# Kernel tuning notes

Hardware: AMD Instinct MI355X
Metric: run time of the kernel (lower is better)

The kernel has to match this reference:

```python
import jax, jax.numpy as jnp
import numpy as np

D = 2048  # input_size
H = 2048  # hidden_size
B = 8192  # batch


def _xavier(key, shape):
    fan_out, fan_in = shape
    limit = float(np.sqrt(6.0 / (fan_in + fan_out)))
    return jax.random.uniform(key, shape, jnp.float32, -limit, limit)


def setup_inputs() -> dict:
    key = jax.random.key(0)
    ks = jax.random.split(key, 20)
    inp = {
        "x": jax.random.normal(ks[0], (B, D), jnp.float32),
        "h0": jax.random.normal(ks[1], (B, H), jnp.float32),
        "c0": jax.random.normal(ks[2], (B, H), jnp.float32),
    }
    names_i = ["W_ii", "W_if", "W_ig", "W_io"]
    names_h = ["W_hi", "W_hf", "W_hg", "W_ho"]
    for i, n in enumerate(names_i):
        inp[n] = _xavier(ks[3 + i], (H, D))
        inp["b" + n[1:]] = jnp.zeros((H,), jnp.float32)
    for i, n in enumerate(names_h):
        inp[n] = _xavier(ks[7 + i], (H, H))
        inp["b" + n[1:]] = jnp.zeros((H,), jnp.float32)
    return inp


def reference(x, h0, c0,
              W_ii, b_ii, W_hi, b_hi,
              W_if, b_if, W_hf, b_hf,
              W_ig, b_ig, W_hg, b_hg,
              W_io, b_io, W_ho, b_ho):
    # Fuse the 8 small GEMMs into two [*, 4H] GEMMs (gate order: i, f, g, o).
    Wx = jnp.concatenate([W_ii, W_if, W_ig, W_io], axis=0)   # [4H, D]
    Wh = jnp.concatenate([W_hi, W_hf, W_hg, W_ho], axis=0)   # [4H, H]
    b = jnp.concatenate([b_ii + b_hi, b_if + b_hf, b_ig + b_hg, b_io + b_ho])
    gates = x @ Wx.T + h0 @ Wh.T + b                         # [B, 4H]
    i_t = jax.nn.sigmoid(gates[:, 0 * H:1 * H])
    f_t = jax.nn.sigmoid(gates[:, 1 * H:2 * H])
    g_t = jnp.tanh(gates[:, 2 * H:3 * H])
    o_t = jax.nn.sigmoid(gates[:, 3 * H:4 * H])
    c_t = f_t * c0 + i_t * g_t
    h_t = o_t * jnp.tanh(c_t)
    return (h_t, c_t)
```

## Files before the change

### kernel.cpp

```cpp
#include <hip/hip_runtime.h>
#include <hip/hip_bf16.h>
#include <cstdint>
#include <cstddef>

#define BATCH 8192
#define DIN   2048
#define HID   2048
#define KDIM  4096
#define NDIM  8192
#define MDIM  8192
#define BH    16777216
#define NT    64

typedef unsigned short u16;
typedef __bf16 bf16x8 __attribute__((ext_vector_type(8)));
typedef float  f32x4  __attribute__((ext_vector_type(4)));

__device__ __forceinline__ u16 f2bf(float f) {
    union { float f; unsigned u; } a; a.f = f;
    unsigned u = a.u;
    unsigned r = u + 0x7FFFu + ((u >> 16) & 1u);
    return (u16)(r >> 16);
}
__device__ __forceinline__ float lo16(unsigned v) {
    union { unsigned u; float f; } a; a.u = v << 16; return a.f;
}
__device__ __forceinline__ float hi16(unsigned v) {
    union { unsigned u; float f; } a; a.u = v & 0xFFFF0000u; return a.f;
}
__device__ __forceinline__ void unpack8(uint4 p, float* f) {
    f[0] = lo16(p.x); f[1] = hi16(p.x);
    f[2] = lo16(p.y); f[3] = hi16(p.y);
    f[4] = lo16(p.z); f[5] = hi16(p.z);
    f[6] = lo16(p.w); f[7] = hi16(p.w);
}
__device__ __forceinline__ float sigm(float x) {
    return 1.0f / (1.0f + __expf(-x));
}
__device__ __forceinline__ float tanh_fast(float x) {
    return 1.0f - 2.0f / (__expf(2.0f * x) + 1.0f);
}
__device__ __forceinline__ void async16(const void* g, void* lds) {
    __builtin_amdgcn_global_load_lds(
        (const __attribute__((address_space(1))) void*)g,
        (__attribute__((address_space(3))) void*)lds,
        16, 0, 0);
}

__global__ __launch_bounds__(256) void cast_A_kernel(
    const float* __restrict__ x, const float* __restrict__ h0,
    u16* __restrict__ Abf)
{
    size_t i8 = ((size_t)blockIdx.x * 256 + threadIdx.x) * 8;
    size_t row = i8 >> 12;
    int col = (int)(i8 & 4095);
    const float* src = (col < DIN) ? (x + row * DIN + col)
                                   : (h0 + row * HID + (col - DIN));
    float4 v0 = ((const float4*)src)[0];
    float4 v1 = ((const float4*)src)[1];
    uint4 o;
    o.x = (unsigned)f2bf(v0.x) | ((unsigned)f2bf(v0.y) << 16);
    o.y = (unsigned)f2bf(v0.z) | ((unsigned)f2bf(v0.w) << 16);
    o.z = (unsigned)f2bf(v1.x) | ((unsigned)f2bf(v1.y) << 16);
    o.w = (unsigned)f2bf(v1.z) | ((unsigned)f2bf(v1.w) << 16);
    *(uint4*)(Abf + i8) = o;
}

__global__ __launch_bounds__(256) void cast_W_kernel(
    const float* __restrict__ Wii, const float* __restrict__ Wif,
    const float* __restrict__ Wig, const float* __restrict__ Wio,
    const float* __restrict__ Whi, const float* __restrict__ Whf,
    const float* __restrict__ Whg, const float* __restrict__ Who,
    u16* __restrict__ Wbf)
{
    size_t i8 = ((size_t)blockIdx.x * 256 + threadIdx.x) * 8;
    size_t n = i8 >> 12;
    int k = (int)(i8 & 4095);
    int gate = (int)(n >> 11);
    size_t h = n & 2047;
    const float* src;
    if (k < DIN) {
        const float* W = (gate == 0) ? Wii : (gate == 1) ? Wif : (gate == 2) ? Wig : Wio;
        src = W + h * DIN + k;
    } else {
        const float* W = (gate == 0) ? Whi : (gate == 1) ? Whf : (gate == 2) ? Whg : Who;
        src = W + h * HID + (k - DIN);
    }
    float4 v0 = ((const float4*)src)[0];
    float4 v1 = ((const float4*)src)[1];
    uint4 o;
    o.x = (unsigned)f2bf(v0.x) | ((unsigned)f2bf(v0.y) << 16);
    o.y = (unsigned)f2bf(v0.z) | ((unsigned)f2bf(v0.w) << 16);
    o.z = (unsigned)f2bf(v1.x) | ((unsigned)f2bf(v1.y) << 16);
    o.w = (unsigned)f2bf(v1.z) | ((unsigned)f2bf(v1.w) << 16);
    *(uint4*)(Wbf + i8) = o;
}

__global__ __launch_bounds__(512, 2) void gemm_lstm_kernel(
    const u16* __restrict__ A,
    const u16* __restrict__ W,
    const float* __restrict__ c0,
    const float* __restrict__ bii, const float* __restrict__ bhi,
    const float* __restrict__ bif, const float* __restrict__ bhf,
    const float* __restrict__ big, const float* __restrict__ bhg,
    const float* __restrict__ bio, const float* __restrict__ bho,
    float* __restrict__ out)
{
    __shared__ u16 SM[65536];

    const int tid  = threadIdx.x;
    const int lane = tid & 63;
    const int wave = tid >> 6;
    const int wm   = wave >> 2;
    const int wn   = wave & 3;
    const int quad = lane >> 4;
    const int l16  = lane & 15;

    const int wg = ((blockIdx.x & 7) << 7) + (blockIdx.x >> 3);
    const size_t m0  = (size_t)(wg >> 5) * 256;
    const size_t hb0 = (size_t)(wg & 31) * 64;

    const int rr = tid >> 3;
    const int gq = (tid & 7) ^ (rr & 7);
    const size_t offA = (m0 + rr) * (size_t)KDIM + (size_t)gq * 8;
    const size_t offB = (hb0 + rr) * (size_t)KDIM + (size_t)gq * 8;
    const int wvb = wave << 10;
    char* AsB = (char*)SM;
    char* BsB = (char*)SM + 65536;

#define STG_A(BUF, J, K0) async16(A + offA + (size_t)(J) * 64 * KDIM + (size_t)(K0), \
                                  AsB + (BUF) * 32768 + (J) * 8192 + wvb)
#define STG_B(BUF, J, K0) async16(W + offB + (size_t)(J) * 2048 * KDIM + (size_t)(K0), \
                                  BsB + (BUF) * 32768 + (J) * 8192 + wvb)

    STG_A(0, 0, 0); STG_A(0, 1, 0); STG_A(0, 2, 0); STG_A(0, 3, 0);
    STG_B(0, 0, 0); STG_B(0, 1, 0); STG_B(0, 2, 0); STG_B(0, 3, 0);
    STG_A(1, 0, 64); STG_A(1, 2, 64);

    f32x4 acc[8][4];
    #pragma unroll
    for (int i = 0; i < 8; ++i)
        #pragma unroll
        for (int j = 0; j < 4; ++j)
            acc[i][j] = (f32x4){0.f, 0.f, 0.f, 0.f};

    const int a_base = (wm * 128 + l16) * 64;
    const int b_base = (wn * 64 + l16) * 64;
    int coff[2];
    coff[0] = (quad * 8) ^ ((l16 & 7) * 8);
    coff[1] = coff[0] ^ 32;

    asm volatile("s_waitcnt vmcnt(2)" ::: "memory");
    __builtin_amdgcn_sched_barrier(0);
    __builtin_amdgcn_s_barrier();

    bf16x8 af[4][2], bfr[2][2];

#define LDA(MH) { _Pragma("unroll") for (int i = 0; i < 4; ++i) {                        \
                    _Pragma("unroll") for (int k = 0; k < 2; ++k)                        \
                      af[i][k] = *(const bf16x8*)&SM[cur * 16384 + a_base + ((MH)*4 + i) * 1024 + coff[k]]; } }
#define LDB(NH) { _Pragma("unroll") for (int j = 0; j < 2; ++j) {                        \
                    _Pragma("unroll") for (int k = 0; k < 2; ++k)                        \
                      bfr[j][k] = *(const bf16x8*)&SM[32768 + cur * 16384 + b_base + ((NH)*2 + j) * 1024 + coff[k]]; } }
#define MM(MH, NH) { __builtin_amdgcn_s_setprio(1);                                      \
                     _Pragma("unroll") for (int k = 0; k < 2; ++k) {                     \
                       _Pragma("unroll") for (int i = 0; i < 4; ++i) {                   \
                         _Pragma("unroll") for (int j = 0; j < 2; ++j)                   \
                           acc[(MH)*4 + i][(NH)*2 + j] =                                 \
                             __builtin_amdgcn_mfma_f32_16x16x32_bf16(                    \
                               af[i][k], bfr[j][k], acc[(MH)*4 + i][(NH)*2 + j], 0, 0, 0); } } \
                     __builtin_amdgcn_s_setprio(0); }

    #pragma unroll 2
    for (int u = 0; u < NT; ++u) {
        const int cur = u & 1;
        const int nxt = cur ^ 1;

        LDA(0); LDB(0);
        if (u + 1 < NT) {
            const int k1 = (u + 1) * 64;
            STG_A(nxt, 1, k1); STG_A(nxt, 3, k1);
            STG_B(nxt, 0, k1); STG_B(nxt, 1, k1);
            STG_B(nxt, 2, k1); STG_B(nxt, 3, k1);
        }
        __builtin_amdgcn_s_barrier();
        MM(0, 0);
        __builtin_amdgcn_s_barrier();

        LDB(1);
        __builtin_amdgcn_s_barrier();
        MM(0, 1);
        __builtin_amdgcn_s_barrier();

        LDA(1); LDB(0);
        if (u + 2 < NT) {
            const int k2 = (u + 2) * 64;
            STG_A(cur, 0, k2); STG_A(cur, 2, k2);
        }
        __builtin_amdgcn_s_barrier();
        MM(1, 0);
        __builtin_amdgcn_s_barrier();

        LDB(1);
        __builtin_amdgcn_s_barrier();
        MM(1, 1);
        if (u < NT - 2) { asm volatile("s_waitcnt vmcnt(2)" ::: "memory"); }
        else            { asm volatile("s_waitcnt vmcnt(0)" ::: "memory"); }
        __builtin_amdgcn_sched_barrier(0);
        __builtin_amdgcn_s_barrier();
    }

#undef STG_A
#undef STG_B
#undef LDA
#undef LDB
#undef MM

    char* smB = (char*)SM;
    #pragma unroll
    for (int mi = 0; mi < 8; ++mi) {
        #pragma unroll
        for (int ni = 0; ni < 4; ++ni) {
            int col  = wn * 64 + ni * 16 + l16;
            int rowb = wm * 128 + mi * 16 + quad * 4;
            int addr = (col * 512 + rowb * 2) ^ ((l16 & 7) << 4);
            uint2 pk;
            pk.x = (unsigned)f2bf(acc[mi][ni][0]) | ((unsigned)f2bf(acc[mi][ni][1]) << 16);
            pk.y = (unsigned)f2bf(acc[mi][ni][2]) | ((unsigned)f2bf(acc[mi][ni][3]) << 16);
            *(uint2*)(smB + addr) = pk;
        }
    }
    __syncthreads();

    {
        const int jj = lane;
        const size_t hg = hb0 + jj;
        float bs0 = bii[hg] + bhi[hg];
        float bs1 = bif[hg] + bhf[hg];
        float bs2 = big[hg] + bhg[hg];
        float bs3 = bio[hg] + bho[hg];
        const int swz = (jj & 7) << 4;

        #pragma unroll
        for (int c = 0; c < 4; ++c) {
            const int r0 = wave * 32 + c * 8;
            float gi[8], gf[8], gg[8], go[8];
            unpack8(*(const uint4*)(smB + (((0 * 64 + jj) * 512 + r0 * 2) ^ swz)), gi);
            unpack8(*(const uint4*)(smB + (((1 * 64 + jj) * 512 + r0 * 2) ^ swz)), gf);
            unpack8(*(const uint4*)(smB + (((2 * 64 + jj) * 512 + r0 * 2) ^ swz)), gg);
            unpack8(*(const uint4*)(smB + (((3 * 64 + jj) * 512 + r0 * 2) ^ swz)), go);
            #pragma unroll
            for (int e = 0; e < 8; ++e) {
                size_t m = m0 + r0 + e;
                float c0v = c0[m * HID + hg];
                float vi = sigm(gi[e] + bs0);
                float vf = sigm(gf[e] + bs1);
                float vg = tanh_fast(gg[e] + bs2);
                float vo = sigm(go[e] + bs3);
                float cc = vf * c0v + vi * vg;
                out[m * HID + hg]      = vo * tanh_fast(cc);
                out[BH + m * HID + hg] = cc;
            }
        }
    }
}

extern "C" void kernel_launch(void* const* d_in, const int* in_sizes, int n_in,
                              void* d_out, int out_size, void* d_ws, size_t ws_size,
                              hipStream_t stream) {
    const float* x   = (const float*)d_in[0];
    const float* h0  = (const float*)d_in[1];
    const float* c0  = (const float*)d_in[2];
    const float* Wii = (const float*)d_in[3];  const float* bii = (const float*)d_in[4];
    const float* Wif = (const float*)d_in[5];  const float* bif = (const float*)d_in[6];
    const float* Wig = (const float*)d_in[7];  const float* big = (const float*)d_in[8];
    const float* Wio = (const float*)d_in[9];  const float* bio = (const float*)d_in[10];
    const float* Whi = (const float*)d_in[11]; const float* bhi = (const float*)d_in[12];
    const float* Whf = (const float*)d_in[13]; const float* bhf = (const float*)d_in[14];
    const float* Whg = (const float*)d_in[15]; const float* bhg = (const float*)d_in[16];
    const float* Who = (const float*)d_in[17]; const float* bho = (const float*)d_in[18];
    float* out = (float*)d_out;

    u16* Abf = (u16*)d_ws;
    u16* Wbf = Abf + (size_t)MDIM * KDIM;

    cast_A_kernel<<<16384, 256, 0, stream>>>(x, h0, Abf);
    cast_W_kernel<<<16384, 256, 0, stream>>>(Wii, Wif, Wig, Wio, Whi, Whf, Whg, Who, Wbf);
    gemm_lstm_kernel<<<1024, 512, 0, stream>>>(Abf, Wbf, c0,
        bii, bhi, bif, bhf, big, bhg, bio, bho, out);
}
```

Measured before the change: 846.1 us.

## Fuse fp32-to-bf16 casts into GEMM via register-staged loads

Removes the two separate cast kernels and the bf16 workspace. The GEMM now loads fp32 x/h0 and weights straight from global memory into registers, converts them to bf16 and writes them into swizzled LDS, with the prefetch interleaved across the four MFMA phases. This avoids a full extra pass over the inputs and the workspace round trip. In exchange the GEMM reads twice as many bytes, because operands are re-fetched as fp32 by many tiles. Registers holding the staged data also raise pressure and replace the async global-to-LDS copies.

Measured after the change: 1.371 ms. 1.62x slower.

```diff
diff --git a/kernel.cpp b/kernel.cpp
--- a/kernel.cpp
+++ b/kernel.cpp
@@ -15,6 +15,7 @@
 typedef unsigned short u16;
 typedef __bf16 bf16x8 __attribute__((ext_vector_type(8)));
 typedef float  f32x4  __attribute__((ext_vector_type(4)));
+typedef float  f32x8  __attribute__((ext_vector_type(8)));
 
 __device__ __forceinline__ u16 f2bf(float f) {
     union { float f; unsigned u; } a; a.f = f;
@@ -40,66 +41,20 @@
 __device__ __forceinline__ float tanh_fast(float x) {
     return 1.0f - 2.0f / (__expf(2.0f * x) + 1.0f);
 }
-__device__ __forceinline__ void async16(const void* g, void* lds) {
-    __builtin_amdgcn_global_load_lds(
-        (const __attribute__((address_space(1))) void*)g,
-        (__attribute__((address_space(3))) void*)lds,
-        16, 0, 0);
-}
-
-__global__ __launch_bounds__(256) void cast_A_kernel(
-    const float* __restrict__ x, const float* __restrict__ h0,
-    u16* __restrict__ Abf)
-{
-    size_t i8 = ((size_t)blockIdx.x * 256 + threadIdx.x) * 8;
-    size_t row = i8 >> 12;
-    int col = (int)(i8 & 4095);
-    const float* src = (col < DIN) ? (x + row * DIN + col)
-                                   : (h0 + row * HID + (col - DIN));
-    float4 v0 = ((const float4*)src)[0];
-    float4 v1 = ((const float4*)src)[1];
-    uint4 o;
-    o.x = (unsigned)f2bf(v0.x) | ((unsigned)f2bf(v0.y) << 16);
-    o.y = (unsigned)f2bf(v0.z) | ((unsigned)f2bf(v0.w) << 16);
-    o.z = (unsigned)f2bf(v1.x) | ((unsigned)f2bf(v1.y) << 16);
-    o.w = (unsigned)f2bf(v1.z) | ((unsigned)f2bf(v1.w) << 16);
-    *(uint4*)(Abf + i8) = o;
-}
-
-__global__ __launch_bounds__(256) void cast_W_kernel(
+__device__ __forceinline__ void cvt_write(void* dst, float4 a, float4 b) {
+    union { float4 q[2]; f32x8 v; } u; u.q[0] = a; u.q[1] = b;
+    bf16x8 o = __builtin_convertvector(u.v, bf16x8);
+    *(bf16x8*)dst = o;
+}
+
+__global__ __launch_bounds__(512, 2) void gemm_lstm_kernel(
+    const float* __restrict__ x,
+    const float* __restrict__ h0,
+    const float* __restrict__ c0,
     const float* __restrict__ Wii, const float* __restrict__ Wif,
     const float* __restrict__ Wig, const float* __restrict__ Wio,
     const float* __restrict__ Whi, const float* __restrict__ Whf,
     const float* __restrict__ Whg, const float* __restrict__ Who,
-    u16* __restrict__ Wbf)
-{
-    size_t i8 = ((size_t)blockIdx.x * 256 + threadIdx.x) * 8;
-    size_t n = i8 >> 12;
-    int k = (int)(i8 & 4095);
-    int gate = (int)(n >> 11);
-    size_t h = n & 2047;
-    const float* src;
-    if (k < DIN) {
-        const float* W = (gate == 0) ? Wii : (gate == 1) ? Wif : (gate == 2) ? Wig : Wio;
-        src = W + h * DIN + k;
-    } else {
-        const float* W = (gate == 0) ? Whi : (gate == 1) ? Whf : (gate == 2) ? Whg : Who;
-        src = W + h * HID + (k - DIN);
-    }
-    float4 v0 = ((const float4*)src)[0];
-    float4 v1 = ((const float4*)src)[1];
-    uint4 o;
-    o.x = (unsigned)f2bf(v0.x) | ((unsigned)f2bf(v0.y) << 16);
-    o.y = (unsigned)f2bf(v0.z) | ((unsigned)f2bf(v0.w) << 16);
-    o.z = (unsigned)f2bf(v1.x) | ((unsigned)f2bf(v1.y) << 16);
-    o.w = (unsigned)f2bf(v1.z) | ((unsigned)f2bf(v1.w) << 16);
-    *(uint4*)(Wbf + i8) = o;
-}
-
-__global__ __launch_bounds__(512, 2) void gemm_lstm_kernel(
-    const u16* __restrict__ A,
-    const u16* __restrict__ W,
-    const float* __restrict__ c0,
     const float* __restrict__ bii, const float* __restrict__ bhi,
     const float* __restrict__ bif, const float* __restrict__ bhf,
     const float* __restrict__ big, const float* __restrict__ bhg,
@@ -120,22 +75,47 @@
     const size_t m0  = (size_t)(wg >> 5) * 256;
     const size_t hb0 = (size_t)(wg & 31) * 64;
 
-    const int rr = tid >> 3;
-    const int gq = (tid & 7) ^ (rr & 7);
-    const size_t offA = (m0 + rr) * (size_t)KDIM + (size_t)gq * 8;
-    const size_t offB = (hb0 + rr) * (size_t)KDIM + (size_t)gq * 8;
-    const int wvb = wave << 10;
-    char* AsB = (char*)SM;
-    char* BsB = (char*)SM + 65536;
-
-#define STG_A(BUF, J, K0) async16(A + offA + (size_t)(J) * 64 * KDIM + (size_t)(K0), \
-                                  AsB + (BUF) * 32768 + (J) * 8192 + wvb)
-#define STG_B(BUF, J, K0) async16(W + offB + (size_t)(J) * 2048 * KDIM + (size_t)(K0), \
-                                  BsB + (BUF) * 32768 + (J) * 8192 + wvb)
-
-    STG_A(0, 0, 0); STG_A(0, 1, 0); STG_A(0, 2, 0); STG_A(0, 3, 0);
-    STG_B(0, 0, 0); STG_B(0, 1, 0); STG_B(0, 2, 0); STG_B(0, 3, 0);
-    STG_A(1, 0, 64); STG_A(1, 2, 64);
+    const int rr  = tid >> 3;
+    const int g8  = (tid & 7) * 8;
+    const int gsw = ((tid & 7) ^ (rr & 7)) * 16;
+    const size_t aoff = (m0 + rr) * 2048 + g8;
+    const size_t boff = (hb0 + rr) * 2048 + g8;
+    char* smB = (char*)SM;
+
+    float4 stA[4], stB0[4], stB1[4];
+
+#define BP0(u2) (((u2) < 32) ? Wii : Whi)
+#define BP1(u2) (((u2) < 32) ? Wif : Whf)
+#define BP2(u2) (((u2) < 32) ? Wig : Whg)
+#define BP3(u2) (((u2) < 32) ? Wio : Who)
+
+#define ISS_A(dst, JA, JB, u2) { \
+    const float* pa_ = (((u2) < 32) ? x : h0) + (((u2) & 31) << 6); \
+    dst[0] = *(const float4*)(pa_ + aoff + (JA) * 131072); \
+    dst[1] = *(const float4*)(pa_ + aoff + (JA) * 131072 + 4); \
+    dst[2] = *(const float4*)(pa_ + aoff + (JB) * 131072); \
+    dst[3] = *(const float4*)(pa_ + aoff + (JB) * 131072 + 4); }
+#define ISS_B01(u2) { \
+    const float* pb0_ = BP0(u2) + (((u2) & 31) << 6); \
+    const float* pb1_ = BP1(u2) + (((u2) & 31) << 6); \
+    stB0[0] = *(const float4*)(pb0_ + boff); \
+    stB0[1] = *(const float4*)(pb0_ + boff + 4); \
+    stB0[2] = *(const float4*)(pb1_ + boff); \
+    stB0[3] = *(const float4*)(pb1_ + boff + 4); }
+#define ISS_B23(u2) { \
+    const float* pb2_ = BP2(u2) + (((u2) & 31) << 6); \
+    const float* pb3_ = BP3(u2) + (((u2) & 31) << 6); \
+    stB1[0] = *(const float4*)(pb2_ + boff); \
+    stB1[1] = *(const float4*)(pb2_ + boff + 4); \
+    stB1[2] = *(const float4*)(pb3_ + boff); \
+    stB1[3] = *(const float4*)(pb3_ + boff + 4); }
+
+#define WRTJ(baseB, J_, q0, q1) \
+    cvt_write(smB + (baseB) + (J_) * 8192 + rr * 128 + gsw, q0, q1)
+#define WRT_A02(BUF) { WRTJ((BUF)*32768, 0, stA[0], stA[1]);  WRTJ((BUF)*32768, 2, stA[2], stA[3]); }
+#define WRT_A13(BUF) { WRTJ((BUF)*32768, 1, stA[0], stA[1]);  WRTJ((BUF)*32768, 3, stA[2], stA[3]); }
+#define WRT_B01(BUF) { WRTJ(65536+(BUF)*32768, 0, stB0[0], stB0[1]); WRTJ(65536+(BUF)*32768, 1, stB0[2], stB0[3]); }
+#define WRT_B23(BUF) { WRTJ(65536+(BUF)*32768, 2, stB1[0], stB1[1]); WRTJ(65536+(BUF)*32768, 3, stB1[2], stB1[3]); }
 
     f32x4 acc[8][4];
     #pragma unroll
@@ -149,10 +129,6 @@
     int coff[2];
     coff[0] = (quad * 8) ^ ((l16 & 7) * 8);
     coff[1] = coff[0] ^ 32;
-
-    asm volatile("s_waitcnt vmcnt(2)" ::: "memory");
-    __builtin_amdgcn_sched_barrier(0);
-    __builtin_amdgcn_s_barrier();
 
     bf16x8 af[4][2], bfr[2][2];
 
@@ -171,52 +147,54 @@
                                af[i][k], bfr[j][k], acc[(MH)*4 + i][(NH)*2 + j], 0, 0, 0); } } \
                      __builtin_amdgcn_s_setprio(0); }
 
+    ISS_A(stA, 0, 2, 0);
+    ISS_B01(0); ISS_B23(0);
+    WRT_A02(0); WRT_B01(0); WRT_B23(0);
+    ISS_A(stA, 1, 3, 0);
+    asm volatile("s_waitcnt lgkmcnt(0)" ::: "memory");
+    __builtin_amdgcn_sched_barrier(0);
+    __builtin_amdgcn_s_barrier();
+
     #pragma unroll 2
     for (int u = 0; u < NT; ++u) {
         const int cur = u & 1;
         const int nxt = cur ^ 1;
-
+        const bool pf = (u + 1 < NT);
+
+        WRT_A13(cur);
         LDA(0); LDB(0);
-        if (u + 1 < NT) {
-            const int k1 = (u + 1) * 64;
-            STG_A(nxt, 1, k1); STG_A(nxt, 3, k1);
-            STG_B(nxt, 0, k1); STG_B(nxt, 1, k1);
-            STG_B(nxt, 2, k1); STG_B(nxt, 3, k1);
-        }
+        if (pf) ISS_A(stA, 0, 2, u + 1);
         __builtin_amdgcn_s_barrier();
         MM(0, 0);
         __builtin_amdgcn_s_barrier();
 
         LDB(1);
+        if (pf) ISS_B01(u + 1);
         __builtin_amdgcn_s_barrier();
         MM(0, 1);
         __builtin_amdgcn_s_barrier();
 
+        if (pf) WRT_A02(nxt);
         LDA(1); LDB(0);
-        if (u + 2 < NT) {
-            const int k2 = (u + 2) * 64;
-            STG_A(cur, 0, k2); STG_A(cur, 2, k2);
-        }
+        if (pf) ISS_B23(u + 1);
         __builtin_amdgcn_s_barrier();
         MM(1, 0);
         __builtin_amdgcn_s_barrier();
 
+        if (pf) { WRT_B01(nxt); WRT_B23(nxt); }
         LDB(1);
+        if (pf) ISS_A(stA, 1, 3, u + 1);
         __builtin_amdgcn_s_barrier();
         MM(1, 1);
-        if (u < NT - 2) { asm volatile("s_waitcnt vmcnt(2)" ::: "memory"); }
-        else            { asm volatile("s_waitcnt vmcnt(0)" ::: "memory"); }
+        asm volatile("s_waitcnt lgkmcnt(0)" ::: "memory");
         __builtin_amdgcn_sched_barrier(0);
         __builtin_amdgcn_s_barrier();
     }
 
-#undef STG_A
-#undef STG_B
 #undef LDA
 #undef LDB
 #undef MM
 
-    char* smB = (char*)SM;
     #pragma unroll
     for (int mi = 0; mi < 8; ++mi) {
         #pragma unroll
@@ -281,11 +259,7 @@
     const float* Who = (const float*)d_in[17]; const float* bho = (const float*)d_in[18];
     float* out = (float*)d_out;
 
-    u16* Abf = (u16*)d_ws;
-    u16* Wbf = Abf + (size_t)MDIM * KDIM;
-
-    cast_A_kernel<<<16384, 256, 0, stream>>>(x, h0, Abf);
-    cast_W_kernel<<<16384, 256, 0, stream>>>(Wii, Wif, Wig, Wio, Whi, Whf, Whg, Who, Wbf);
-    gemm_lstm_kernel<<<1024, 512, 0, stream>>>(Abf, Wbf, c0,
+    gemm_lstm_kernel<<<1024, 512, 0, stream>>>(x, h0, c0,
+        Wii, Wif, Wig, Wio, Whi, Whf, Whg, Who,
         bii, bhi, bif, bhf, big, bhg, bio, bho, out);
 }
```
